# Kernel optimization log

Hardware: AMD Instinct MI355X
Metric: run time of the kernel (lower is better)

The kernel has to match this reference:

```python
import jax, jax.numpy as jnp
import numpy as np

STRIDE = (4, 4)
MASK = (17, 17)
G_MEAN = 85.384
G_STD = 53.798
LEV = 5  # len(bins)
EPS = 1e-8
_BINS = np.array([0.0, 0.5, G_MEAN - G_STD, G_MEAN, G_MEAN + G_STD], dtype=np.float32)
_DISTS = [1, 2, 4]
_THETAS = [0.0, np.pi / 4, np.pi / 2, 3 * np.pi / 4]
# skimage greycomatrix offsets: (row, col) = (round(sin(t)*d), round(cos(t)*d)), dist-major
OFFSETS = [(int(round(np.sin(t) * d)), int(round(np.cos(t) * d))) for d in _DISTS for t in _THETAS]


def setup_inputs():
    key = jax.random.key(0)
    x = jax.random.uniform(key, (8, 1, 512, 512), dtype=jnp.float32) * 255.0
    return {"inputs": x}


def _sliding_windows(x):
    B, C, H, W = x.shape
    nx = (H - MASK[0]) // STRIDE[0] + 1
    ny = (W - MASK[1]) // STRIDE[1] + 1
    rows = (jnp.arange(nx) * STRIDE[0])[:, None] + jnp.arange(MASK[0])  # (nx, Mx)
    cols = (jnp.arange(ny) * STRIDE[1])[:, None] + jnp.arange(MASK[1])  # (ny, My)
    w = x[:, :, rows]              # (B, C, nx, Mx, W)
    w = w[:, :, :, :, cols]        # (B, C, nx, Mx, ny, My)
    return jnp.transpose(w, (0, 1, 2, 4, 3, 5))  # (B, C, nx, ny, Mx, My)


def _statistics(w):
    m = w.mean(axis=(-2, -1))
    s = w.std(axis=(-2, -1))
    mx = w.max(axis=(-2, -1))
    mn = w.min(axis=(-2, -1))
    # Faithful to original: mean is rescaled in-place BEFORE being used in max/min stats
    m = m / G_MEAN
    s = s / G_STD
    mx = (mx - m) / G_STD
    mn = (m - mn) / G_STD
    return jnp.concatenate([m, s, mx, mn], axis=1)  # (B, 4*C, nx, ny)


def _glcm(qf, dr, dc):
    # qf: (Wn, Mx, My) int32 -> normalized symmetric GLCM (Wn, LEV, LEV)
    Mx, My = qf.shape[-2:]
    if dc >= 0:
        a = qf[:, :Mx - dr, :My - dc]
        b = qf[:, dr:, dc:]
    else:
        a = qf[:, :Mx - dr, -dc:]
        b = qf[:, dr:, :My + dc]
    Wn = qf.shape[0]
    code = (a * LEV + b).reshape(Wn, -1)
    flat = (jnp.arange(Wn, dtype=jnp.int32)[:, None] * (LEV * LEV) + code).reshape(-1)
    cnt = jax.ops.segment_sum(jnp.ones(flat.shape, jnp.float32), flat, num_segments=Wn * LEV * LEV)
    G = cnt.reshape(Wn, LEV, LEV)
    G = G + jnp.swapaxes(G, -1, -2)  # symmetric=True
    return G / jnp.sum(G, axis=(-2, -1), keepdims=True)  # normed=True


def _hist_glcm_features(q):
    # q: (B, C, nx, ny, Mx, My) int32 -> (B, 64, nx, ny) (C must be 1)
    B, C, nx, ny, Mx, My = q.shape
    qf = q.reshape(-1, Mx, My)
    Wn = qf.shape[0]
    G = jnp.stack([_glcm(qf, dr, dc) for dr, dc in OFFSETS], axis=1)  # (Wn, 12, L, L)

    I = jnp.arange(LEV, dtype=jnp.float32)
    d2 = (I[:, None] - I[None, :]) ** 2
    contrast = jnp.einsum('wkij,ij->wk', G, d2)
    homogeneity = jnp.einsum('wkij,ij->wk', G, 1.0 / (1.0 + d2))
    energy = jnp.sqrt(jnp.sum(G * G, axis=(-2, -1)))
    Pi = G.sum(axis=-1)   # (Wn, 12, L)
    Pj = G.sum(axis=-2)
    mu_i = jnp.sum(I * Pi, axis=-1)
    mu_j = jnp.sum(I * Pj, axis=-1)
    di = I[None, None, :] - mu_i[..., None]
    dj = I[None, None, :] - mu_j[..., None]
    std_i = jnp.sqrt(jnp.sum(Pi * di * di, axis=-1))
    std_j = jnp.sqrt(jnp.sum(Pj * dj * dj, axis=-1))
    cov = jnp.einsum('wkij,wki,wkj->wk', G, di, dj)
    denom = std_i * std_j
    correlation = jnp.where(denom < 1e-15, 1.0, cov / jnp.maximum(denom, 1e-30))
    entropy = -jnp.sum(G * jnp.log2(G + EPS), axis=(-2, -1))  # (Wn, 12)

    qv = qf.reshape(Wn, -1)
    cnts = jnp.stack([jnp.sum(qv == k, axis=-1) for k in range(1, LEV)], axis=-1).astype(jnp.float32)
    tot = cnts.sum(axis=-1, keepdims=True)
    hist = jnp.where(tot > 0, cnts / jnp.maximum(tot, 1.0), 0.0)  # (Wn, LEV-1)

    feat = jnp.concatenate([hist, contrast, homogeneity, energy, correlation, entropy], axis=-1)
    feat = feat.reshape(B, C, nx, ny, -1)
    return jnp.transpose(feat, (0, 4, 2, 3, 1))[..., 0]  # (B, 64, nx, ny)


def reference(inputs):
    w = _sliding_windows(inputs)                                   # (B,C,nx,ny,17,17)
    stat = _statistics(w)                                          # (B,4,nx,ny)
    q = (jnp.digitize(w, jnp.asarray(_BINS)) - 1).astype(jnp.int32)
    hg = _hist_glcm_features(q)                                    # (B,64,nx,ny)
    feats = jnp.concatenate([stat, hg], axis=1)                    # (B,68,nx,ny)
    return jnp.mean(feats, axis=(-2, -1))                          # (B,68)
```

## Files before the change

kernel.cpp:

```cpp
#include <hip/hip_runtime.h>


#define G_MEAN_F 85.384f
#define G_STD_F  53.798f
#define MASK_WS_BYTES (8u * 512u * 36u * 8u)

__device__ constexpr int LO15[15] = {0,0,0,0,0,1,1,1,1,2,2,2,3,3,4};
__device__ constexpr int HI15[15] = {0,1,2,3,4,1,2,3,4,2,3,4,3,4,4};

__device__ __forceinline__ float wred(float v) {
#pragma unroll
  for (int m = 32; m; m >>= 1) v += __shfl_xor(v, m, 64);
  return v;
}

__device__ __forceinline__ void load_sl(const unsigned* sl, int idx, unsigned m[5]) {
  const uint4 q = *(const uint4*)(sl + idx * 4);
  m[1] = q.x; m[2] = q.y; m[3] = q.z; m[4] = q.w;
  m[0] = 0x1FFFFu & ~(m[1] | m[2] | m[3] | m[4]);
}

template<int DC>
__device__ __forceinline__ void updoff(unsigned* cnt, const unsigned a[5], const unsigned b[5]) {
  unsigned as[5], bs[5];
#pragma unroll
  for (int v = 0; v < 5; ++v) {
    as[v] = (DC < 0) ? (a[v] >> (-DC)) : a[v];
    bs[v] = (DC > 0) ? (b[v] >> DC) : b[v];
  }
#pragma unroll
  for (int u = 0; u < 15; ++u) {
    const int i = LO15[u], j = HI15[u];
    unsigned t = as[i] & bs[j];
    if (i != j) t |= as[j] & bs[i];
    cnt[u] += __popc(t);
  }
}

__device__ __forceinline__ void feat5(const unsigned* cnt, float Np,
                                      float& con, float& hom, float& ene,
                                      float& corr, float& ent) {
  const float invN = 1.0f / Np;
  const float inv2N = 0.5f / Np;
  con = 0.0f; hom = 0.0f; ent = 0.0f;
  float eac = 0.0f;
  float P[5] = {0, 0, 0, 0, 0};
#pragma unroll
  for (int u = 0; u < 15; ++u) {
    const int lo = LO15[u], hi = HI15[u];
    const float m = (float)cnt[u];
    const float d2 = (float)((hi - lo) * (hi - lo));
    con += m * d2;
    hom += m * (1.0f / (1.0f + d2));
    if (lo == hi) {
      eac += m * m;
      P[lo] += 2.0f * m;
      float g = m * invN;
      ent -= g * __log2f(g + 1e-8f);
    } else {
      eac += 0.5f * m * m;
      P[lo] += m; P[hi] += m;
      float g = m * inv2N;
      ent -= 2.0f * g * __log2f(g + 1e-8f);
    }
  }
  con *= invN;
  hom *= invN;
  ene = sqrtf(eac) * invN;
  float mu = 0.0f;
#pragma unroll
  for (int i = 0; i < 5; ++i) { P[i] *= inv2N; mu += (float)i * P[i]; }
  float s2 = 0.0f;
#pragma unroll
  for (int i = 0; i < 5; ++i) { float d = (float)i - mu; s2 = fmaf(P[i] * d, d, s2); }
  float denom = s2;
  float cov = 0.0f;
#pragma unroll
  for (int u = 0; u < 15; ++u)
    cov += ((float)cnt[u] * invN) * ((float)LO15[u] - mu) * ((float)HI15[u] - mu);
  corr = (denom < 1e-15f) ? 1.0f : cov / fmaxf(denom, 1e-30f);
}

__device__ __forceinline__ void emit2(const unsigned c1[15], const unsigned c2[15], float Np,
                                      bool v1, bool v2, float* pt0, int k0, int k1) {
  float con1, hom1, ene1, cor1, ent1, con2, hom2, ene2, cor2, ent2;
  feat5(c1, Np, con1, hom1, ene1, cor1, ent1);
  feat5(c2, Np, con2, hom2, ene2, cor2, ent2);
  if (!v1) { con1 = 0; hom1 = 0; ene1 = 0; cor1 = 0; ent1 = 0; }
  if (!v2) { con2 = 0; hom2 = 0; ene2 = 0; cor2 = 0; ent2 = 0; }
  float con = wred(con1 + con2), hom = wred(hom1 + hom2), ene = wred(ene1 + ene2);
  float cor = wred(cor1 + cor2), ent = wred(ent1 + ent2);
  if ((threadIdx.x & 63) == 0) {
    const float s = 1.0f / 15376.0f;
    pt0[(8 + k0) * 128] = con * s;
    pt0[(20 + k0) * 128] = hom * s;
    pt0[(32 + k0) * 128] = ene * s;
    pt0[(44 + k0) * 128] = cor * s;
    pt0[(56 + k0) * 128] = ent * s;
    if (k1 >= 0) {
      pt0[(8 + k1) * 128] = con * s;
      pt0[(20 + k1) * 128] = hom * s;
      pt0[(32 + k1) * 128] = ene * s;
      pt0[(44 + k1) * 128] = cor * s;
      pt0[(56 + k1) * 128] = ent * s;
    }
  }
}

template<int DR, int DC>
__device__ void glcm2(const unsigned* sl, int s, int ly, bool v1, bool v2,
                      float Np, float* pt0, int k0, int k1) {
  unsigned A[15], S[15], B[15];
#pragma unroll
  for (int u = 0; u < 15; ++u) { A[u] = 0; S[u] = 0; B[u] = 0; }
  unsigned buf[DR > 0 ? DR : 1][5];
  if constexpr (DR > 0) {
#pragma unroll
    for (int i = 0; i < DR; ++i) load_sl(sl, (s + i) * 8 + ly, buf[i]);
  }
  unsigned nxt[5];
  load_sl(sl, (s + DR) * 8 + ly, nxt);

#define SEGRUN(CNT, RB, RE)                                              \
  _Pragma("unroll 1")                                                    \
  for (int R = (RB); R < (RE); ++R) {                                    \
    unsigned cur[5];                                                     \
    _Pragma("unroll")                                                    \
    for (int v = 0; v < 5; ++v) cur[v] = nxt[v];                         \
    load_sl(sl, (s + DR + R + 1) * 8 + ly, nxt);  \
    if constexpr (DR > 0) {                                              \
      updoff<DC>(CNT, buf[0], cur);                                      \
      _Pragma("unroll")                                                  \
      for (int i = 0; i < DR - 1; ++i)                                   \
        _Pragma("unroll")                                                \
        for (int v = 0; v < 5; ++v) buf[i][v] = buf[i + 1][v];           \
      _Pragma("unroll")                                                  \
      for (int v = 0; v < 5; ++v) buf[DR > 0 ? DR - 1 : 0][v] = cur[v];  \
    } else {                                                             \
      updoff<DC>(CNT, cur, cur);                                         \
    }                                                                    \
  }

  SEGRUN(A, 0, 4)
  SEGRUN(S, 4, 17 - DR)
  SEGRUN(B, 17 - DR, 21 - DR)
#undef SEGRUN

#pragma unroll
  for (int u = 0; u < 15; ++u) { A[u] += S[u]; B[u] += S[u]; }
  emit2(A, B, Np, v1, v2, pt0, k0, k1);
}

__global__ __launch_bounds__(64)
void mask_build_kernel(const float* __restrict__ x, unsigned long long* __restrict__ mg) {
  const int lane = threadIdx.x;
  const int r = blockIdx.x;
  const int b = blockIdx.y;
  const float* xr = x + ((size_t)b * 512 + r) * 512;
  unsigned long long* mr = mg + ((size_t)b * 512 + r) * 36;

  const float T1 = 0.5f;
  const float T2 = (float)(85.384 - 53.798);
  const float T3 = 85.384f;
  const float T4 = (float)(85.384 + 53.798);

#pragma unroll 1
  for (int seg = 0; seg < 8; ++seg) {
    float xv = xr[seg * 64 + lane];
    int q = (int)(xv >= T1) + (int)(xv >= T2) + (int)(xv >= T3) + (int)(xv >= T4);
    unsigned long long b1 = __ballot(q == 1);
    unsigned long long b2 = __ballot(q == 2);
    unsigned long long b3 = __ballot(q == 3);
    unsigned long long b4 = __ballot(q == 4);
    if (lane < 4) {
      unsigned long long bv = (lane == 0) ? b1 : (lane == 1) ? b2 : (lane == 2) ? b3 : b4;
      mr[seg * 4 + lane] = bv;
    }
  }
  if (lane < 4) mr[32 + lane] = 0;
}

__global__ __launch_bounds__(768)
void glcm_feat_kernel(const float* __restrict__ x,
                      const unsigned long long* __restrict__ mg,
                      float* __restrict__ part) {
  __shared__ __align__(16) unsigned sl[79 * 8 * 4];

  const int tid = threadIdx.x;
  const int lane = tid & 63;
  const int wid = tid >> 6;
  const int ty = blockIdx.x;
  const int tx = blockIdx.y;
  const int b = blockIdx.z;
  const int px0 = tx * 64;
  const int py0 = ty * 32;
  const float* xb = x + (size_t)b * 512 * 512;

  const int s0 = py0 >> 6;
  const int sh = py0 & 63;
  const unsigned long long* mgb = mg + (size_t)b * 512 * 36 + s0 * 4;
#pragma unroll 1
  for (int t = tid; t < 79 * 8; t += 768) {
    const int row = t >> 3, ly = t & 7;
    unsigned sv[4] = {0, 0, 0, 0};
    if (row < 77) {
      int gr = px0 + row; if (gr > 511) gr = 511;
      const unsigned long long* p = mgb + (size_t)gr * 36;
#pragma unroll
      for (int lev = 0; lev < 4; ++lev) {
        unsigned long long cmb = p[lev];
        if (sh) cmb = (cmb >> 32) | (p[4 + lev] << 32);
        sv[lev] = (unsigned)(cmb >> (4 * ly)) & 0x1FFFFu;
      }
    }
    *(uint4*)(sl + t * 4) = make_uint4(sv[0], sv[1], sv[2], sv[3]);
  }
  __syncthreads();

  const int lxp = lane >> 3, ly = lane & 7;
  const int wx1 = tx * 16 + 2 * lxp;
  const int wy = ty * 8 + ly;
  const bool vy = (wy < 124);
  const bool v1 = (wx1 < 124) && vy;
  const bool v2 = (wx1 + 1 < 124) && vy;
  const int s = 8 * lxp;
  const int tile = tx * 16 + ty;
  float* pt0 = part + (size_t)b * 68 * 128 + tile;

  if (wid == 0) {
    int sp = px0 + s; if (sp > 488) sp = 488;
    int c0 = py0 + 4 * ly; if (c0 > 492) c0 = 492;
    const float* fw = xb + (size_t)sp * 512 + c0;
    float sA = 0, qA = 0, sS = 0, qS = 0, sB = 0, qB = 0;
    float mxA = -1e30f, mnA = 1e30f, mxS = -1e30f, mnS = 1e30f, mxB = -1e30f, mnB = 1e30f;
#pragma unroll 1
    for (int r = 0; r < 21; ++r) {
      const float* p = fw + r * 512;
      const float4* p4 = (const float4*)p;
      float rs = 0, rq = 0, rmx = -1e30f, rmn = 1e30f;
#pragma unroll
      for (int w = 0; w < 4; ++w) {
        float4 f = p4[w];
        rs += f.x; rq = fmaf(f.x, f.x, rq); rmx = fmaxf(rmx, f.x); rmn = fminf(rmn, f.x);
        rs += f.y; rq = fmaf(f.y, f.y, rq); rmx = fmaxf(rmx, f.y); rmn = fminf(rmn, f.y);
        rs += f.z; rq = fmaf(f.z, f.z, rq); rmx = fmaxf(rmx, f.z); rmn = fminf(rmn, f.z);
        rs += f.w; rq = fmaf(f.w, f.w, rq); rmx = fmaxf(rmx, f.w); rmn = fminf(rmn, f.w);
      }
      float t = p[16];
      rs += t; rq = fmaf(t, t, rq); rmx = fmaxf(rmx, t); rmn = fminf(rmn, t);
      if (r < 4)       { sA += rs; qA += rq; mxA = fmaxf(mxA, rmx); mnA = fminf(mnA, rmn); }
      else if (r < 17) { sS += rs; qS += rq; mxS = fmaxf(mxS, rmx); mnS = fminf(mnS, rmn); }
      else             { sB += rs; qB += rq; mxB = fmaxf(mxB, rmx); mnB = fminf(mnB, rmn); }
    }
    float ch[4][2];
#pragma unroll
    for (int w = 0; w < 2; ++w) {
      float sum = w ? (sS + sB) : (sA + sS);
      float ssq = w ? (qS + qB) : (qA + qS);
      float mx = w ? fmaxf(mxS, mxB) : fmaxf(mxA, mxS);
      float mn = w ? fminf(mnS, mnB) : fminf(mnA, mnS);
      float mean = sum * (1.0f / 289.0f);
      float var = fmaxf(ssq * (1.0f / 289.0f) - mean * mean, 0.0f);
      float fm = mean / G_MEAN_F;
      ch[0][w] = fm;
      ch[1][w] = sqrtf(var) / G_STD_F;
      ch[2][w] = (mx - fm) / G_STD_F;
      ch[3][w] = (fm - mn) / G_STD_F;
    }
#pragma unroll
    for (int c = 0; c < 4; ++c) {
      float f = (v1 ? ch[c][0] : 0.0f) + (v2 ? ch[c][1] : 0.0f);
      f = wred(f);
      if (lane == 0) pt0[c * 128] = f * (1.0f / 15376.0f);
    }
  } else if (wid == 1) {
    unsigned hA[4] = {0,0,0,0}, hS[4] = {0,0,0,0}, hB[4] = {0,0,0,0};
#pragma unroll 1
    for (int R = 0; R < 21; ++R) {
      const uint4 q = *(const uint4*)(sl + ((s + R) * 8 + ly) * 4);
      unsigned* h = (R < 4) ? hA : (R < 17) ? hS : hB;
      h[0] += __popc(q.x); h[1] += __popc(q.y); h[2] += __popc(q.z); h[3] += __popc(q.w);
    }
    float ch[4][2];
#pragma unroll
    for (int w = 0; w < 2; ++w) {
      unsigned t1 = w ? (hS[0] + hB[0]) : (hA[0] + hS[0]);
      unsigned t2 = w ? (hS[1] + hB[1]) : (hA[1] + hS[1]);
      unsigned t3 = w ? (hS[2] + hB[2]) : (hA[2] + hS[2]);
      unsigned t4 = w ? (hS[3] + hB[3]) : (hA[3] + hS[3]);
      unsigned tot = t1 + t2 + t3 + t4;
      float ti = (tot > 0) ? 1.0f / (float)tot : 0.0f;
      ch[0][w] = (float)t1 * ti;
      ch[1][w] = (float)t2 * ti;
      ch[2][w] = (float)t3 * ti;
      ch[3][w] = (float)t4 * ti;
    }
#pragma unroll
    for (int c = 0; c < 4; ++c) {
      float f = (v1 ? ch[c][0] : 0.0f) + (v2 ? ch[c][1] : 0.0f);
      f = wred(f);
      if (lane == 0) pt0[(4 + c) * 128] = f * (1.0f / 15376.0f);
    }
  } else if (wid == 2) {
    glcm2<0, 1>(sl, s, ly, v1, v2, 272.0f, pt0, 0, -1);
  } else if (wid == 3) {
    glcm2<1, 0>(sl, s, ly, v1, v2, 272.0f, pt0, 2, -1);
  } else if (wid == 4) {
    glcm2<0, 2>(sl, s, ly, v1, v2, 255.0f, pt0, 4, -1);
  } else if (wid == 5) {
    glcm2<1, 1>(sl, s, ly, v1, v2, 256.0f, pt0, 1, 5);
  } else if (wid == 6) {
    glcm2<0, 4>(sl, s, ly, v1, v2, 221.0f, pt0, 8, -1);
  } else if (wid == 7) {
    glcm2<1, -1>(sl, s, ly, v1, v2, 256.0f, pt0, 3, 7);
  } else if (wid == 8) {
    glcm2<2, 0>(sl, s, ly, v1, v2, 255.0f, pt0, 6, -1);
  } else if (wid == 9) {
    glcm2<3, 3>(sl, s, ly, v1, v2, 196.0f, pt0, 9, -1);
  } else if (wid == 10) {
    glcm2<4, 0>(sl, s, ly, v1, v2, 221.0f, pt0, 10, -1);
  } else {
    glcm2<3, -3>(sl, s, ly, v1, v2, 196.0f, pt0, 11, -1);
  }
}

__global__ __launch_bounds__(64)
void reduce_kernel(const float* __restrict__ part, float* __restrict__ out) {
  const int ch = blockIdx.x;
  const int b = blockIdx.y;
  const int lane = threadIdx.x;
  const float2* p = (const float2*)(part + ((size_t)b * 68 + ch) * 128);
  float2 f = p[lane];
  float v = f.x + f.y;
  v = wred(v);
  if (lane == 0) out[b * 68 + ch] = v;
}

extern "C" void kernel_launch(void* const* d_in, const int* in_sizes, int n_in,
                              void* d_out, int out_size, void* d_ws, size_t ws_size,
                              hipStream_t stream)
{
  const float* x = (const float*)d_in[0];
  float* out = (float*)d_out;
  unsigned long long* mg = (unsigned long long*)d_ws;
  float* part = (float*)((char*)d_ws + MASK_WS_BYTES);

  mask_build_kernel<<<dim3(512, 8), dim3(64), 0, stream>>>(x, mg);
  glcm_feat_kernel<<<dim3(16, 8, 8), dim3(768), 0, stream>>>(x, mg, part);
  reduce_kernel<<<dim3(68, 8), dim3(64), 0, stream>>>(part, out);
}
```

Before: 109.5 us.

## Fuse quantization bitmask build into GLCM kernel, drop separate mask pass

Removes the standalone mask_build_kernel and its global workspace. Each GLCM block now quantizes its own input tile rows directly from x with ballots and writes the per-level 17-bit window masks into shared memory. This saves one kernel launch and the global round-trip of the mask buffer. In exchange, overlapping tiles re-read and re-quantize halo rows redundantly.

```diff
diff --git a/kernel.cpp b/kernel.cpp
--- a/kernel.cpp
+++ b/kernel.cpp
@@ -3,7 +3,6 @@
 
 #define G_MEAN_F 85.384f
 #define G_STD_F  53.798f
-#define MASK_WS_BYTES (8u * 512u * 36u * 8u)
 
 __device__ constexpr int LO15[15] = {0,0,0,0,0,1,1,1,1,2,2,2,3,3,4};
 __device__ constexpr int HI15[15] = {0,1,2,3,4,1,2,3,4,2,3,4,3,4,4};
@@ -151,38 +150,8 @@
   emit2(A, B, Np, v1, v2, pt0, k0, k1);
 }
 
-__global__ __launch_bounds__(64)
-void mask_build_kernel(const float* __restrict__ x, unsigned long long* __restrict__ mg) {
-  const int lane = threadIdx.x;
-  const int r = blockIdx.x;
-  const int b = blockIdx.y;
-  const float* xr = x + ((size_t)b * 512 + r) * 512;
-  unsigned long long* mr = mg + ((size_t)b * 512 + r) * 36;
-
-  const float T1 = 0.5f;
-  const float T2 = (float)(85.384 - 53.798);
-  const float T3 = 85.384f;
-  const float T4 = (float)(85.384 + 53.798);
-
-#pragma unroll 1
-  for (int seg = 0; seg < 8; ++seg) {
-    float xv = xr[seg * 64 + lane];
-    int q = (int)(xv >= T1) + (int)(xv >= T2) + (int)(xv >= T3) + (int)(xv >= T4);
-    unsigned long long b1 = __ballot(q == 1);
-    unsigned long long b2 = __ballot(q == 2);
-    unsigned long long b3 = __ballot(q == 3);
-    unsigned long long b4 = __ballot(q == 4);
-    if (lane < 4) {
-      unsigned long long bv = (lane == 0) ? b1 : (lane == 1) ? b2 : (lane == 2) ? b3 : b4;
-      mr[seg * 4 + lane] = bv;
-    }
-  }
-  if (lane < 4) mr[32 + lane] = 0;
-}
-
 __global__ __launch_bounds__(768)
 void glcm_feat_kernel(const float* __restrict__ x,
-                      const unsigned long long* __restrict__ mg,
                       float* __restrict__ part) {
   __shared__ __align__(16) unsigned sl[79 * 8 * 4];
 
@@ -196,24 +165,36 @@
   const int py0 = ty * 32;
   const float* xb = x + (size_t)b * 512 * 512;
 
-  const int s0 = py0 >> 6;
-  const int sh = py0 & 63;
-  const unsigned long long* mgb = mg + (size_t)b * 512 * 36 + s0 * 4;
+  const float T1 = 0.5f;
+  const float T2 = (float)(85.384 - 53.798);
+  const float T3 = 85.384f;
+  const float T4 = (float)(85.384 + 53.798);
+
+  {
+    const int col = py0 + lane;
+    const int colc = col > 511 ? 511 : col;
 #pragma unroll 1
-  for (int t = tid; t < 79 * 8; t += 768) {
-    const int row = t >> 3, ly = t & 7;
-    unsigned sv[4] = {0, 0, 0, 0};
-    if (row < 77) {
+    for (int row = wid; row < 77; row += 12) {
       int gr = px0 + row; if (gr > 511) gr = 511;
-      const unsigned long long* p = mgb + (size_t)gr * 36;
-#pragma unroll
-      for (int lev = 0; lev < 4; ++lev) {
-        unsigned long long cmb = p[lev];
-        if (sh) cmb = (cmb >> 32) | (p[4 + lev] << 32);
-        sv[lev] = (unsigned)(cmb >> (4 * ly)) & 0x1FFFFu;
+      const float xv = xb[(size_t)gr * 512 + colc];
+      const int q = (int)(xv >= T1) + (int)(xv >= T2) + (int)(xv >= T3) + (int)(xv >= T4);
+      const bool act = (lane < 45) && (col < 512);
+      const unsigned long long b1 = __ballot(act && q == 1);
+      const unsigned long long b2 = __ballot(act && q == 2);
+      const unsigned long long b3 = __ballot(act && q == 3);
+      const unsigned long long b4 = __ballot(act && q == 4);
+      if (lane < 8) {
+        const int sh4 = 4 * lane;
+        const unsigned s0 = (unsigned)(b1 >> sh4) & 0x1FFFFu;
+        const unsigned s1 = (unsigned)(b2 >> sh4) & 0x1FFFFu;
+        const unsigned s2 = (unsigned)(b3 >> sh4) & 0x1FFFFu;
+        const unsigned s3 = (unsigned)(b4 >> sh4) & 0x1FFFFu;
+        *(uint4*)(sl + (row * 8 + lane) * 4) = make_uint4(s0, s1, s2, s3);
       }
     }
-    *(uint4*)(sl + t * 4) = make_uint4(sv[0], sv[1], sv[2], sv[3]);
+  }
+  if (tid < 16) {
+    *(uint4*)(sl + (77 * 8 + tid) * 4) = make_uint4(0u, 0u, 0u, 0u);
   }
   __syncthreads();
 
@@ -342,10 +323,8 @@
 {
   const float* x = (const float*)d_in[0];
   float* out = (float*)d_out;
-  unsigned long long* mg = (unsigned long long*)d_ws;
-  float* part = (float*)((char*)d_ws + MASK_WS_BYTES);
-
-  mask_build_kernel<<<dim3(512, 8), dim3(64), 0, stream>>>(x, mg);
-  glcm_feat_kernel<<<dim3(16, 8, 8), dim3(768), 0, stream>>>(x, mg, part);
+  float* part = (float*)d_ws;
+
+  glcm_feat_kernel<<<dim3(16, 8, 8), dim3(768), 0, stream>>>(x, part);
   reduce_kernel<<<dim3(68, 8), dim3(64), 0, stream>>>(part, out);
 }
```

New measurement: 111.1 us. Within noise of the previous version (+1.4%).
